# Kernel tuning notes

Hardware: AMD Instinct MI355X
Metric: run time of the kernel (lower is better)

## Reference

```python
import jax, jax.numpy as jnp
import numpy as np

BINS = 8
EPS = 1e-12  # torch F.normalize default eps


def _pairwise_scores(matf):
    # torch: input1[a,b]=matf[b]; transpose(0,1)->matf[a]; transpose(-2,-1)->matf[a]^T [M,F]
    # matmul with input1[a,b]=matf[b] -> scores[a,b] = matf[a]^T @ matf[b], shape [M,M]
    bs, F, M = matf.shape
    s = jnp.einsum('afm,bfn->abmn', matf, matf)  # [bs, bs, M, M]
    return s.reshape(bs * bs, M * M)


def _histc_rows(x, bins):
    # torch.histc semantics with min=max=0: range = [row.min(), row.max()],
    # values == max land in the last bin.
    mn = jnp.min(x, axis=1, keepdims=True)
    mx = jnp.max(x, axis=1, keepdims=True)
    denom = jnp.where(mx > mn, mx - mn, jnp.ones_like(mx))
    idx = jnp.clip(jnp.floor((x - mn) / denom * bins).astype(jnp.int32), 0, bins - 1)
    nbs = x.shape[0]
    flat = (idx + (jnp.arange(nbs, dtype=jnp.int32) * bins)[:, None]).ravel()
    h = jnp.zeros(nbs * bins, dtype=x.dtype).at[flat].add(1.0)
    return h.reshape(nbs, bins)


def _l2_normalize(h):
    n = jnp.linalg.norm(h, axis=-1, keepdims=True)
    return h / jnp.maximum(n, EPS)


def setup_inputs() -> dict:
    key = jax.random.key(0)
    k1, k2 = jax.random.split(key)
    bs, F, M = 64, 256, 128
    matf1 = jax.random.normal(k1, (bs, F, M), dtype=jnp.float32)
    matf2 = jax.random.normal(k2, (bs, F, M), dtype=jnp.float32)
    return {"matf1": matf1, "matf2": matf2}


def reference(matf1, matf2):
    # scores are .detach()ed in the original; stop_gradient for faithfulness
    scores1 = jax.lax.stop_gradient(_pairwise_scores(matf1))  # [nbs, M*M]
    scores2 = jax.lax.stop_gradient(_pairwise_scores(matf2))
    h1 = _l2_normalize(_histc_rows(scores1, BINS))  # [nbs, 8]
    h2 = _l2_normalize(_histc_rows(scores2, BINS))
    return jnp.concatenate([h1, h2], axis=-1)  # [nbs, 16]
```

## Files before the change

### kernel.cpp

```cpp
#include <hip/hip_runtime.h>
#include <math.h>

#define BS 64
#define F  256
#define M  128
#define MF (M * F)
#define NBP 1056

typedef unsigned short u16;
typedef _Float16 f16x8 __attribute__((ext_vector_type(8)));
typedef float    f32x16 __attribute__((ext_vector_type(16)));

__global__ __launch_bounds__(256) void convert_f16_kernel(
    const float* __restrict__ m1, const float* __restrict__ m2,
    u16* __restrict__ hT)
{
    __shared__ float tile[64 * M];
    const int mat = blockIdx.x >> 6;
    const int b   = blockIdx.x & 63;
    const int f0  = blockIdx.y * 64;
    const float* src = (mat == 0 ? m1 : m2) + (size_t)b * MF + (size_t)f0 * M;
    const int tid = threadIdx.x;

    const float4* g = (const float4*)src;
    float4* s = (float4*)tile;
    #pragma unroll
    for (int i = 0; i < 8; ++i)
        s[tid + i * 256] = g[tid + i * 256];
    __syncthreads();

    const size_t obase = ((size_t)(mat * BS + b) * 32 + (f0 >> 3)) * 1024;
    #pragma unroll
    for (int it = 0; it < 4; ++it) {
        const int idx = it * 256 + tid;
        const int f8l = idx >> 7;
        const int m   = idx & 127;
        u16 hh[8] __attribute__((aligned(16)));
        #pragma unroll
        for (int j = 0; j < 8; ++j) {
            const float x = tile[(f8l * 8 + j) * M + m];
            const _Float16 h = (_Float16)x;
            hh[j] = __builtin_bit_cast(u16, h);
        }
        *(uint4*)&hT[obase + (size_t)idx * 8] = *(const uint4*)hh;
    }
}

__global__ __launch_bounds__(256, 2) void gram_hist_mfma(
    const u16* __restrict__ hT, float* __restrict__ out)
{
    __shared__ u16 lds[2 * 4096];
    __shared__ float smin[4], smax[4];
    __shared__ int hist[2][8];

    const int tid  = threadIdx.x;
    const int lane = tid & 63;
    const int w    = tid >> 6;

    if (tid < 16) hist[tid >> 3][tid & 7] = 0;

    int p = blockIdx.x, a = 0;
    { int cnt = 32; while (p >= cnt) { p -= cnt; ++a; cnt = (64 - a + 1) >> 1; } }
    const int b1 = a + 2 * p;
    int b2 = b1 + 1;
    const bool b2valid = (b2 <= 63);
    if (!b2valid) b2 = b1;
    const int mat = blockIdx.y;

    const int pp = w >> 1;
    const int c  = w & 1;
    const int l31   = lane & 31;
    const int lhalf = lane >> 5;

    const u16* pa = hT + (size_t)(mat * BS + a) * MF + tid * 8;
    const int d0 = tid * 8;
    const int d1 = (256 + tid) * 8;

    const int bsel = pp ? b2 : b1;
    const u16* pb = hT + (size_t)(mat * BS + bsel) * MF
                  + (size_t)(lhalf * 1024 + c * 512 + l31 * 8);

    f32x16 acc[4][2];
    #pragma unroll
    for (int ti = 0; ti < 4; ++ti)
        #pragma unroll
        for (int u = 0; u < 2; ++u)
            #pragma unroll
            for (int r = 0; r < 16; ++r) acc[ti][u][r] = 0.0f;

    f16x8 bc[2][2], bn[2][2];

    uint4 r0 = *(const uint4*)(pa);
    uint4 r1 = *(const uint4*)(pa + 2048);
    #pragma unroll
    for (int kk = 0; kk < 2; ++kk)
        #pragma unroll
        for (int t = 0; t < 2; ++t)
            bc[kk][t] = *(const f16x8*)(pb + kk * 2048 + t * 256);
    *(uint4*)&lds[d0] = r0;
    *(uint4*)&lds[d1] = r1;
    __syncthreads();

    for (int it = 0; it < 8; ++it) {
        const int cur = (it & 1) * 4096;
        const int alt = cur ^ 4096;

        if (it < 7) {
            const int koff = (it + 1) * 4096;
            r0 = *(const uint4*)(pa + koff);
            r1 = *(const uint4*)(pa + koff + 2048);
            #pragma unroll
            for (int kk = 0; kk < 2; ++kk)
                #pragma unroll
                for (int t = 0; t < 2; ++t)
                    bn[kk][t] = *(const f16x8*)(pb + koff + kk * 2048 + t * 256);
        }

        #pragma unroll
        for (int kk = 0; kk < 2; ++kk) {
            const int kb = kk * 2 + lhalf;
            f16x8 af[4];
            #pragma unroll
            for (int t = 0; t < 4; ++t)
                af[t] = *(const f16x8*)&lds[cur + (kb * 128 + t * 32 + l31) * 8];
            #pragma unroll
            for (int ti = 0; ti < 4; ++ti)
                #pragma unroll
                for (int u = 0; u < 2; ++u)
                    acc[ti][u] = __builtin_amdgcn_mfma_f32_32x32x16_f16(af[ti], bc[kk][u], acc[ti][u], 0, 0, 0);
        }

        if (it < 7) {
            *(uint4*)&lds[alt + d0] = r0;
            *(uint4*)&lds[alt + d1] = r1;
            #pragma unroll
            for (int kk = 0; kk < 2; ++kk)
                #pragma unroll
                for (int t = 0; t < 2; ++t)
                    bc[kk][t] = bn[kk][t];
        }
        __syncthreads();
    }

    float vmin = acc[0][0][0], vmax = vmin;
    #pragma unroll
    for (int ti = 0; ti < 4; ++ti)
        #pragma unroll
        for (int u = 0; u < 2; ++u)
            #pragma unroll
            for (int r = 0; r < 16; ++r) {
                vmin = fminf(vmin, acc[ti][u][r]);
                vmax = fmaxf(vmax, acc[ti][u][r]);
            }
    #pragma unroll
    for (int off = 1; off < 64; off <<= 1) {
        vmin = fminf(vmin, __shfl_xor(vmin, off, 64));
        vmax = fmaxf(vmax, __shfl_xor(vmax, off, 64));
    }
    if (lane == 0) { smin[w] = vmin; smax[w] = vmax; }
    __syncthreads();
    const float pmn = fminf(smin[pp * 2], smin[pp * 2 + 1]);
    const float pmx = fmaxf(smax[pp * 2], smax[pp * 2 + 1]);
    const float denom = (pmx > pmn) ? (pmx - pmn) : 1.0f;
    const float scale = 8.0f / denom;
    const float bias  = -pmn * scale;

    unsigned w0 = 0, w1 = 0;
    #pragma unroll
    for (int ti = 0; ti < 4; ++ti)
        #pragma unroll
        for (int u = 0; u < 2; ++u)
            #pragma unroll
            for (int r = 0; r < 16; ++r) {
                const float t = fmaf(acc[ti][u][r], scale, bias);
                int k = (int)t;
                k = k > 7 ? 7 : k;
                const unsigned inc = 1u << ((k & 3) * 8);
                if (k < 4) w0 += inc; else w1 += inc;
            }
    unsigned e0 = (w0 & 0xFFu)         | (((w0 >> 8)  & 0xFFu) << 16);
    unsigned e1 = ((w0 >> 16) & 0xFFu) | (((w0 >> 24) & 0xFFu) << 16);
    unsigned e2 = (w1 & 0xFFu)         | (((w1 >> 8)  & 0xFFu) << 16);
    unsigned e3 = ((w1 >> 16) & 0xFFu) | (((w1 >> 24) & 0xFFu) << 16);
    #pragma unroll
    for (int off = 32; off > 0; off >>= 1) {
        e0 += __shfl_down(e0, off, 64);
        e1 += __shfl_down(e1, off, 64);
        e2 += __shfl_down(e2, off, 64);
        e3 += __shfl_down(e3, off, 64);
    }
    if (lane == 0) {
        atomicAdd(&hist[pp][0], (int)(e0 & 0xFFFFu)); atomicAdd(&hist[pp][1], (int)(e0 >> 16));
        atomicAdd(&hist[pp][2], (int)(e1 & 0xFFFFu)); atomicAdd(&hist[pp][3], (int)(e1 >> 16));
        atomicAdd(&hist[pp][4], (int)(e2 & 0xFFFFu)); atomicAdd(&hist[pp][5], (int)(e2 >> 16));
        atomicAdd(&hist[pp][6], (int)(e3 & 0xFFFFu)); atomicAdd(&hist[pp][7], (int)(e3 >> 16));
    }
    __syncthreads();

    const int B = (pp == 0) ? b1 : b2;
    const bool valid = (pp == 0) || b2valid;
    if (valid && c == 0 && lane < 8) {
        float ss = 0.0f;
        #pragma unroll
        for (int k = 0; k < 8; ++k) {
            const float cc = (float)hist[pp][k];
            ss += cc * cc;
        }
        const float nrm = fmaxf(sqrtf(ss), 1e-12f);
        const float v = (float)hist[pp][lane] / nrm;
        out[((size_t)a * BS + B) * 16 + mat * 8 + lane] = v;
        if (a != B)
            out[((size_t)B * BS + a) * 16 + mat * 8 + lane] = v;
    }
}

extern "C" void kernel_launch(void* const* d_in, const int* in_sizes, int n_in,
                              void* d_out, int out_size, void* d_ws, size_t ws_size,
                              hipStream_t stream) {
    const float* m1 = (const float*)d_in[0];
    const float* m2 = (const float*)d_in[1];
    float* out = (float*)d_out;

    u16* hT = (u16*)d_ws;

    convert_f16_kernel<<<dim3(128, 4), 256, 0, stream>>>(m1, m2, hT);
    gram_hist_mfma<<<dim3(NBP, 2), 256, 0, stream>>>(hT, out);
}
```

Measured before the change: 114.9 us.

## Split gram tile across eight waves and unroll double-buffered K loop

Each block now runs 512 threads (8 waves) instead of 256, and each wave computes a 64x64 sub-tile (2x2 MFMAs) rather than 128x64, which halves accumulator registers per wave. The aim is higher occupancy and more waves to hide global and LDS latency. The K loop is fully unrolled into explicit ping-pong phases with macros, and each thread now stages one A vector per step. The cost is more waves sharing the same LDS data and the per-block min/max reduction now spanning 4 waves per pair.

```diff
diff --git a/kernel.cpp b/kernel.cpp
--- a/kernel.cpp
+++ b/kernel.cpp
@@ -46,11 +46,35 @@
     }
 }
 
-__global__ __launch_bounds__(256, 2) void gram_hist_mfma(
+
+#define LOADB(DST, CH) {                                      \
+    const u16* pbk = pb + (CH) * 4096;                        \
+    DST[0][0] = *(const f16x8*)(pbk);                         \
+    DST[0][1] = *(const f16x8*)(pbk + 256);                   \
+    DST[1][0] = *(const f16x8*)(pbk + 2048);                  \
+    DST[1][1] = *(const f16x8*)(pbk + 2048 + 256);            \
+}
+
+#define MFMA_PHASE(CUR, BF) {                                                                   \
+    const f16x8 a00 = *(const f16x8*)&lds[(CUR) + aoff];                                        \
+    const f16x8 a01 = *(const f16x8*)&lds[(CUR) + aoff + 256];                                  \
+    acc[0][0] = __builtin_amdgcn_mfma_f32_32x32x16_f16(a00, BF[0][0], acc[0][0], 0, 0, 0);      \
+    acc[0][1] = __builtin_amdgcn_mfma_f32_32x32x16_f16(a00, BF[0][1], acc[0][1], 0, 0, 0);      \
+    acc[1][0] = __builtin_amdgcn_mfma_f32_32x32x16_f16(a01, BF[0][0], acc[1][0], 0, 0, 0);      \
+    acc[1][1] = __builtin_amdgcn_mfma_f32_32x32x16_f16(a01, BF[0][1], acc[1][1], 0, 0, 0);      \
+    const f16x8 a10 = *(const f16x8*)&lds[(CUR) + 2048 + aoff];                                 \
+    const f16x8 a11 = *(const f16x8*)&lds[(CUR) + 2048 + aoff + 256];                           \
+    acc[0][0] = __builtin_amdgcn_mfma_f32_32x32x16_f16(a10, BF[1][0], acc[0][0], 0, 0, 0);      \
+    acc[0][1] = __builtin_amdgcn_mfma_f32_32x32x16_f16(a10, BF[1][1], acc[0][1], 0, 0, 0);      \
+    acc[1][0] = __builtin_amdgcn_mfma_f32_32x32x16_f16(a11, BF[1][0], acc[1][0], 0, 0, 0);      \
+    acc[1][1] = __builtin_amdgcn_mfma_f32_32x32x16_f16(a11, BF[1][1], acc[1][1], 0, 0, 0);      \
+}
+
+__global__ __launch_bounds__(512, 4) void gram_hist_mfma(
     const u16* __restrict__ hT, float* __restrict__ out)
 {
     __shared__ u16 lds[2 * 4096];
-    __shared__ float smin[4], smax[4];
+    __shared__ float smin[8], smax[8];
     __shared__ int hist[2][8];
 
     const int tid  = threadIdx.x;
@@ -67,84 +91,64 @@
     if (!b2valid) b2 = b1;
     const int mat = blockIdx.y;
 
-    const int pp = w >> 1;
-    const int c  = w & 1;
+    const int pp = w >> 2;
+    const int rh = (w >> 1) & 1;
+    const int ch = w & 1;
     const int l31   = lane & 31;
     const int lhalf = lane >> 5;
 
     const u16* pa = hT + (size_t)(mat * BS + a) * MF + tid * 8;
     const int d0 = tid * 8;
-    const int d1 = (256 + tid) * 8;
+
+    const int aoff = lhalf * 1024 + (rh * 64 + l31) * 8;
 
     const int bsel = pp ? b2 : b1;
     const u16* pb = hT + (size_t)(mat * BS + bsel) * MF
-                  + (size_t)(lhalf * 1024 + c * 512 + l31 * 8);
-
-    f32x16 acc[4][2];
-    #pragma unroll
-    for (int ti = 0; ti < 4; ++ti)
+                  + (size_t)(lhalf * 1024 + ch * 512 + l31 * 8);
+
+    f32x16 acc[2][2];
+    #pragma unroll
+    for (int ti = 0; ti < 2; ++ti)
         #pragma unroll
         for (int u = 0; u < 2; ++u)
             #pragma unroll
             for (int r = 0; r < 16; ++r) acc[ti][u][r] = 0.0f;
 
-    f16x8 bc[2][2], bn[2][2];
-
-    uint4 r0 = *(const uint4*)(pa);
-    uint4 r1 = *(const uint4*)(pa + 2048);
-    #pragma unroll
-    for (int kk = 0; kk < 2; ++kk)
-        #pragma unroll
-        for (int t = 0; t < 2; ++t)
-            bc[kk][t] = *(const f16x8*)(pb + kk * 2048 + t * 256);
-    *(uint4*)&lds[d0] = r0;
-    *(uint4*)&lds[d1] = r1;
-    __syncthreads();
-
-    for (int it = 0; it < 8; ++it) {
-        const int cur = (it & 1) * 4096;
-        const int alt = cur ^ 4096;
-
-        if (it < 7) {
-            const int koff = (it + 1) * 4096;
-            r0 = *(const uint4*)(pa + koff);
-            r1 = *(const uint4*)(pa + koff + 2048);
-            #pragma unroll
-            for (int kk = 0; kk < 2; ++kk)
-                #pragma unroll
-                for (int t = 0; t < 2; ++t)
-                    bn[kk][t] = *(const f16x8*)(pb + koff + kk * 2048 + t * 256);
-        }
-
-        #pragma unroll
-        for (int kk = 0; kk < 2; ++kk) {
-            const int kb = kk * 2 + lhalf;
-            f16x8 af[4];
-            #pragma unroll
-            for (int t = 0; t < 4; ++t)
-                af[t] = *(const f16x8*)&lds[cur + (kb * 128 + t * 32 + l31) * 8];
-            #pragma unroll
-            for (int ti = 0; ti < 4; ++ti)
-                #pragma unroll
-                for (int u = 0; u < 2; ++u)
-                    acc[ti][u] = __builtin_amdgcn_mfma_f32_32x32x16_f16(af[ti], bc[kk][u], acc[ti][u], 0, 0, 0);
-        }
-
-        if (it < 7) {
-            *(uint4*)&lds[alt + d0] = r0;
-            *(uint4*)&lds[alt + d1] = r1;
-            #pragma unroll
-            for (int kk = 0; kk < 2; ++kk)
-                #pragma unroll
-                for (int t = 0; t < 2; ++t)
-                    bc[kk][t] = bn[kk][t];
-        }
-        __syncthreads();
+    uint4 rA;
+    f16x8 bA[2][2], bB[2][2];
+
+    rA = *(const uint4*)pa;
+    LOADB(bA, 0);
+    *(uint4*)&lds[d0] = rA;
+    __syncthreads();
+
+    #pragma unroll
+    for (int itp = 0; itp < 4; ++itp) {
+        {
+            const int nxt = 2 * itp + 1;
+            rA = *(const uint4*)(pa + nxt * 4096);
+            LOADB(bB, nxt);
+            MFMA_PHASE(0, bA);
+            *(uint4*)&lds[4096 + d0] = rA;
+            __syncthreads();
+        }
+        {
+            if (itp < 3) {
+                const int nxt = 2 * itp + 2;
+                rA = *(const uint4*)(pa + nxt * 4096);
+                LOADB(bA, nxt);
+            }
+            MFMA_PHASE(4096, bB);
+            if (itp < 3) {
+                *(uint4*)&lds[d0] = rA;
+                __syncthreads();
+            }
+        }
     }
 
     float vmin = acc[0][0][0], vmax = vmin;
     #pragma unroll
-    for (int ti = 0; ti < 4; ++ti)
+    for (int ti = 0; ti < 2; ++ti)
         #pragma unroll
         for (int u = 0; u < 2; ++u)
             #pragma unroll
@@ -159,15 +163,18 @@
     }
     if (lane == 0) { smin[w] = vmin; smax[w] = vmax; }
     __syncthreads();
-    const float pmn = fminf(smin[pp * 2], smin[pp * 2 + 1]);
-    const float pmx = fmaxf(smax[pp * 2], smax[pp * 2 + 1]);
+    const int pb4 = pp * 4;
+    const float pmn = fminf(fminf(smin[pb4], smin[pb4 + 1]),
+                            fminf(smin[pb4 + 2], smin[pb4 + 3]));
+    const float pmx = fmaxf(fmaxf(smax[pb4], smax[pb4 + 1]),
+                            fmaxf(smax[pb4 + 2], smax[pb4 + 3]));
     const float denom = (pmx > pmn) ? (pmx - pmn) : 1.0f;
     const float scale = 8.0f / denom;
     const float bias  = -pmn * scale;
 
     unsigned w0 = 0, w1 = 0;
     #pragma unroll
-    for (int ti = 0; ti < 4; ++ti)
+    for (int ti = 0; ti < 2; ++ti)
         #pragma unroll
         for (int u = 0; u < 2; ++u)
             #pragma unroll
@@ -199,7 +206,7 @@
 
     const int B = (pp == 0) ? b1 : b2;
     const bool valid = (pp == 0) || b2valid;
-    if (valid && c == 0 && lane < 8) {
+    if (valid && rh == 0 && ch == 0 && lane < 8) {
         float ss = 0.0f;
         #pragma unroll
         for (int k = 0; k < 8; ++k) {
@@ -224,5 +231,5 @@
     u16* hT = (u16*)d_ws;
 
     convert_f16_kernel<<<dim3(128, 4), 256, 0, stream>>>(m1, m2, hT);
-    gram_hist_mfma<<<dim3(NBP, 2), 256, 0, stream>>>(hT, out);
-}
+    gram_hist_mfma<<<dim3(NBP, 2), 512, 0, stream>>>(hT, out);
+}
```

After: 117.7 us. +2.4%, slower.

## Stage full A operand in LDS once and ping-pong B register prefetch

Applied to the files above, without the earlier changes.

Instead of double-buffering the shared A matrix through LDS in eight K-chunks, each with a barrier, the kernel now loads the whole 128x256 f16 A tile (64 KB) into LDS up front behind a single barrier. The K loop is fully unrolled with two B register sets that alternate, so the next chunk's global loads overlap the current chunk's MFMAs. This removes seven per-iteration barriers and LDS store phases, at the cost of a much larger shared-memory footprint that may reduce how many blocks fit per CU, plus a longer exposed load before compute starts.

```diff
diff --git a/kernel.cpp b/kernel.cpp
--- a/kernel.cpp
+++ b/kernel.cpp
@@ -46,10 +46,39 @@
     }
 }
 
+
+#define LOADB(DST, IT) {                                      \
+    const u16* pbk = pb + (IT) * 4096;                        \
+    DST[0][0] = *(const f16x8*)(pbk);                         \
+    DST[0][1] = *(const f16x8*)(pbk + 256);                   \
+    DST[1][0] = *(const f16x8*)(pbk + 2048);                  \
+    DST[1][1] = *(const f16x8*)(pbk + 2048 + 256);            \
+}
+
+#define MFMA_CHUNK(IT, BF) {                                                                        \
+    f16x8 af[4];                                                                                    \
+    _Pragma("unroll")                                                                               \
+    for (int t = 0; t < 4; ++t)                                                                     \
+        af[t] = *(const f16x8*)&lds[(IT) * 4096 + t * 256 + abase];                                 \
+    _Pragma("unroll")                                                                               \
+    for (int ti = 0; ti < 4; ++ti) {                                                                \
+        acc[ti][0] = __builtin_amdgcn_mfma_f32_32x32x16_f16(af[ti], BF[0][0], acc[ti][0], 0, 0, 0); \
+        acc[ti][1] = __builtin_amdgcn_mfma_f32_32x32x16_f16(af[ti], BF[0][1], acc[ti][1], 0, 0, 0); \
+    }                                                                                               \
+    _Pragma("unroll")                                                                               \
+    for (int t = 0; t < 4; ++t)                                                                     \
+        af[t] = *(const f16x8*)&lds[(IT) * 4096 + 2048 + t * 256 + abase];                          \
+    _Pragma("unroll")                                                                               \
+    for (int ti = 0; ti < 4; ++ti) {                                                                \
+        acc[ti][0] = __builtin_amdgcn_mfma_f32_32x32x16_f16(af[ti], BF[1][0], acc[ti][0], 0, 0, 0); \
+        acc[ti][1] = __builtin_amdgcn_mfma_f32_32x32x16_f16(af[ti], BF[1][1], acc[ti][1], 0, 0, 0); \
+    }                                                                                               \
+}
+
 __global__ __launch_bounds__(256, 2) void gram_hist_mfma(
     const u16* __restrict__ hT, float* __restrict__ out)
 {
-    __shared__ u16 lds[2 * 4096];
+    __shared__ u16 lds[32768];
     __shared__ float smin[4], smax[4];
     __shared__ int hist[2][8];
 
@@ -72,14 +101,14 @@
     const int l31   = lane & 31;
     const int lhalf = lane >> 5;
 
-    const u16* pa = hT + (size_t)(mat * BS + a) * MF + tid * 8;
-    const int d0 = tid * 8;
-    const int d1 = (256 + tid) * 8;
-
     const int bsel = pp ? b2 : b1;
     const u16* pb = hT + (size_t)(mat * BS + bsel) * MF
                   + (size_t)(lhalf * 1024 + c * 512 + l31 * 8);
 
+    const u16* pa = hT + (size_t)(mat * BS + a) * MF + tid * 8;
+
+    const int abase = lhalf * 1024 + l31 * 8;
+
     f32x16 acc[4][2];
     #pragma unroll
     for (int ti = 0; ti < 4; ++ti)
@@ -88,58 +117,23 @@
             #pragma unroll
             for (int r = 0; r < 16; ++r) acc[ti][u][r] = 0.0f;
 
-    f16x8 bc[2][2], bn[2][2];
-
-    uint4 r0 = *(const uint4*)(pa);
-    uint4 r1 = *(const uint4*)(pa + 2048);
-    #pragma unroll
-    for (int kk = 0; kk < 2; ++kk)
-        #pragma unroll
-        for (int t = 0; t < 2; ++t)
-            bc[kk][t] = *(const f16x8*)(pb + kk * 2048 + t * 256);
-    *(uint4*)&lds[d0] = r0;
-    *(uint4*)&lds[d1] = r1;
-    __syncthreads();
-
-    for (int it = 0; it < 8; ++it) {
-        const int cur = (it & 1) * 4096;
-        const int alt = cur ^ 4096;
-
-        if (it < 7) {
-            const int koff = (it + 1) * 4096;
-            r0 = *(const uint4*)(pa + koff);
-            r1 = *(const uint4*)(pa + koff + 2048);
-            #pragma unroll
-            for (int kk = 0; kk < 2; ++kk)
-                #pragma unroll
-                for (int t = 0; t < 2; ++t)
-                    bn[kk][t] = *(const f16x8*)(pb + koff + kk * 2048 + t * 256);
-        }
-
-        #pragma unroll
-        for (int kk = 0; kk < 2; ++kk) {
-            const int kb = kk * 2 + lhalf;
-            f16x8 af[4];
-            #pragma unroll
-            for (int t = 0; t < 4; ++t)
-                af[t] = *(const f16x8*)&lds[cur + (kb * 128 + t * 32 + l31) * 8];
-            #pragma unroll
-            for (int ti = 0; ti < 4; ++ti)
-                #pragma unroll
-                for (int u = 0; u < 2; ++u)
-                    acc[ti][u] = __builtin_amdgcn_mfma_f32_32x32x16_f16(af[ti], bc[kk][u], acc[ti][u], 0, 0, 0);
-        }
-
-        if (it < 7) {
-            *(uint4*)&lds[alt + d0] = r0;
-            *(uint4*)&lds[alt + d1] = r1;
-            #pragma unroll
-            for (int kk = 0; kk < 2; ++kk)
-                #pragma unroll
-                for (int t = 0; t < 2; ++t)
-                    bc[kk][t] = bn[kk][t];
-        }
-        __syncthreads();
+    f16x8 bA[2][2], bB[2][2];
+
+    LOADB(bA, 0);
+
+    #pragma unroll
+    for (int i = 0; i < 16; ++i) {
+        const uint4 v = *(const uint4*)(pa + i * 2048);
+        *(uint4*)&lds[(tid + i * 256) * 8] = v;
+    }
+    __syncthreads();
+
+    #pragma unroll
+    for (int itp = 0; itp < 4; ++itp) {
+        LOADB(bB, 2 * itp + 1);
+        MFMA_CHUNK(2 * itp, bA);
+        if (itp < 3) LOADB(bA, 2 * itp + 2);
+        MFMA_CHUNK(2 * itp + 1, bB);
     }
 
     float vmin = acc[0][0][0], vmax = vmin;
```

After: 116.1 us. No clear change (+1.0%).

## Unroll double-buffered K loop with ping-pong B registers and XCD-aware block mapping

Applied to the files above, without the earlier changes.

The main K loop is unrolled by two, and B fragments now ping-pong between two register sets, which removes the register copy and the runtime buffer-offset arithmetic. The last iteration also drops its barrier. The launch grid is flattened to 1D, and block IDs are remapped so that each group of four XCDs handles one matrix with contiguous pair ranges, aiming to improve L2 reuse of the A and B rows. The extra register set raises register pressure and could hurt occupancy at two blocks per CU.

```diff
diff --git a/kernel.cpp b/kernel.cpp
--- a/kernel.cpp
+++ b/kernel.cpp
@@ -46,6 +46,15 @@
     }
 }
 
+
+#define LOADB(DST, CH) {                                      \
+    const u16* pbk = pb + (CH) * 4096;                        \
+    DST[0][0] = *(const f16x8*)(pbk);                         \
+    DST[0][1] = *(const f16x8*)(pbk + 256);                   \
+    DST[1][0] = *(const f16x8*)(pbk + 2048);                  \
+    DST[1][1] = *(const f16x8*)(pbk + 2048 + 256);            \
+}
+
 __global__ __launch_bounds__(256, 2) void gram_hist_mfma(
     const u16* __restrict__ hT, float* __restrict__ out)
 {
@@ -59,13 +68,16 @@
 
     if (tid < 16) hist[tid >> 3][tid & 7] = 0;
 
-    int p = blockIdx.x, a = 0;
+    const int bid  = blockIdx.x;
+    const int xcd  = bid & 7;
+    const int mat  = xcd >> 2;
+    int p = (xcd & 3) * 264 + (bid >> 3);
+    int a = 0;
     { int cnt = 32; while (p >= cnt) { p -= cnt; ++a; cnt = (64 - a + 1) >> 1; } }
     const int b1 = a + 2 * p;
     int b2 = b1 + 1;
     const bool b2valid = (b2 <= 63);
     if (!b2valid) b2 = b1;
-    const int mat = blockIdx.y;
 
     const int pp = w >> 1;
     const int c  = w & 1;
@@ -88,58 +100,69 @@
             #pragma unroll
             for (int r = 0; r < 16; ++r) acc[ti][u][r] = 0.0f;
 
-    f16x8 bc[2][2], bn[2][2];
-
-    uint4 r0 = *(const uint4*)(pa);
-    uint4 r1 = *(const uint4*)(pa + 2048);
-    #pragma unroll
-    for (int kk = 0; kk < 2; ++kk)
-        #pragma unroll
-        for (int t = 0; t < 2; ++t)
-            bc[kk][t] = *(const f16x8*)(pb + kk * 2048 + t * 256);
+    uint4 r0, r1;
+    f16x8 bA[2][2], bB[2][2];
+
+    r0 = *(const uint4*)(pa);
+    r1 = *(const uint4*)(pa + 2048);
+    LOADB(bA, 0);
     *(uint4*)&lds[d0] = r0;
     *(uint4*)&lds[d1] = r1;
     __syncthreads();
 
-    for (int it = 0; it < 8; ++it) {
-        const int cur = (it & 1) * 4096;
-        const int alt = cur ^ 4096;
-
-        if (it < 7) {
-            const int koff = (it + 1) * 4096;
-            r0 = *(const uint4*)(pa + koff);
-            r1 = *(const uint4*)(pa + koff + 2048);
-            #pragma unroll
-            for (int kk = 0; kk < 2; ++kk)
-                #pragma unroll
-                for (int t = 0; t < 2; ++t)
-                    bn[kk][t] = *(const f16x8*)(pb + koff + kk * 2048 + t * 256);
-        }
-
-        #pragma unroll
-        for (int kk = 0; kk < 2; ++kk) {
-            const int kb = kk * 2 + lhalf;
-            f16x8 af[4];
-            #pragma unroll
-            for (int t = 0; t < 4; ++t)
-                af[t] = *(const f16x8*)&lds[cur + (kb * 128 + t * 32 + l31) * 8];
-            #pragma unroll
-            for (int ti = 0; ti < 4; ++ti)
-                #pragma unroll
-                for (int u = 0; u < 2; ++u)
-                    acc[ti][u] = __builtin_amdgcn_mfma_f32_32x32x16_f16(af[ti], bc[kk][u], acc[ti][u], 0, 0, 0);
-        }
-
-        if (it < 7) {
-            *(uint4*)&lds[alt + d0] = r0;
-            *(uint4*)&lds[alt + d1] = r1;
-            #pragma unroll
-            for (int kk = 0; kk < 2; ++kk)
-                #pragma unroll
-                for (int t = 0; t < 2; ++t)
-                    bc[kk][t] = bn[kk][t];
-        }
-        __syncthreads();
+    #pragma unroll
+    for (int itp = 0; itp < 4; ++itp) {
+        {
+            const int nxt = 2 * itp + 1;
+            r0 = *(const uint4*)(pa + nxt * 4096);
+            r1 = *(const uint4*)(pa + nxt * 4096 + 2048);
+            LOADB(bB, nxt);
+
+            const int cur = 0;
+            #pragma unroll
+            for (int kk = 0; kk < 2; ++kk) {
+                const int base = cur + kk * 2048 + lhalf * 1024 + l31 * 8;
+                f16x8 af[4];
+                #pragma unroll
+                for (int t = 0; t < 4; ++t)
+                    af[t] = *(const f16x8*)&lds[base + t * 256];
+                #pragma unroll
+                for (int ti = 0; ti < 4; ++ti) {
+                    acc[ti][0] = __builtin_amdgcn_mfma_f32_32x32x16_f16(af[ti], bA[kk][0], acc[ti][0], 0, 0, 0);
+                    acc[ti][1] = __builtin_amdgcn_mfma_f32_32x32x16_f16(af[ti], bA[kk][1], acc[ti][1], 0, 0, 0);
+                }
+            }
+            *(uint4*)&lds[4096 + d0] = r0;
+            *(uint4*)&lds[4096 + d1] = r1;
+            __syncthreads();
+        }
+        {
+            if (itp < 3) {
+                const int nxt = 2 * itp + 2;
+                r0 = *(const uint4*)(pa + nxt * 4096);
+                r1 = *(const uint4*)(pa + nxt * 4096 + 2048);
+                LOADB(bA, nxt);
+            }
+            const int cur = 4096;
+            #pragma unroll
+            for (int kk = 0; kk < 2; ++kk) {
+                const int base = cur + kk * 2048 + lhalf * 1024 + l31 * 8;
+                f16x8 af[4];
+                #pragma unroll
+                for (int t = 0; t < 4; ++t)
+                    af[t] = *(const f16x8*)&lds[base + t * 256];
+                #pragma unroll
+                for (int ti = 0; ti < 4; ++ti) {
+                    acc[ti][0] = __builtin_amdgcn_mfma_f32_32x32x16_f16(af[ti], bB[kk][0], acc[ti][0], 0, 0, 0);
+                    acc[ti][1] = __builtin_amdgcn_mfma_f32_32x32x16_f16(af[ti], bB[kk][1], acc[ti][1], 0, 0, 0);
+                }
+            }
+            if (itp < 3) {
+                *(uint4*)&lds[d0] = r0;
+                *(uint4*)&lds[d1] = r1;
+                __syncthreads();
+            }
+        }
     }
 
     float vmin = acc[0][0][0], vmax = vmin;
@@ -224,5 +247,5 @@
     u16* hT = (u16*)d_ws;
 
     convert_f16_kernel<<<dim3(128, 4), 256, 0, stream>>>(m1, m2, hT);
-    gram_hist_mfma<<<dim3(NBP, 2), 256, 0, stream>>>(hT, out);
-}
+    gram_hist_mfma<<<2 * NBP, 256, 0, stream>>>(hT, out);
+}
```

After: 115.0 us. No clear change (+0.1%).
